# Optimization experiments

Hardware: AMD Instinct MI355X
Metric: run time of the kernel (lower is better)

The kernel has to match this reference:

```python
import jax, jax.numpy as jnp
from jax import lax
import numpy as np

B, C_IN, H, W = 8, 64, 128, 128
C_OUT, K = 64, 3
STRIDE, PAD, DIL = 1, 1, 1
KK = K * K
H_OUT = (H + 2 * PAD - DIL * (K - 1) - 1) // STRIDE + 1
W_OUT = (W + 2 * PAD - DIL * (K - 1) - 1) // STRIDE + 1


def setup_inputs() -> dict:
    key = jax.random.key(0)
    k1, k2, k3, k4 = jax.random.split(key, 4)
    x = jax.random.normal(k1, (B, C_IN, H, W), jnp.float32)
    # offset-predicting conv params (zero-init in the module; use small random
    # values so the deformable sampling path is actually exercised)
    offset_w = jax.random.normal(k2, (2 * KK, C_IN, K, K), jnp.float32) * 0.01
    offset_b = jax.random.normal(k3, (2 * KK,), jnp.float32) * 0.01
    weight = jax.random.normal(k4, (C_OUT, C_IN, K, K), jnp.float32) * (1.0 / np.sqrt(C_IN * KK))
    return {"x": x, "offset_w": offset_w, "offset_b": offset_b, "weight": weight}


def reference(x, offset_w, offset_b, weight):
    # 1) predict offsets: [B, 2*K*K, Hout, Wout], layout (dy, dx) per kernel tap
    offset = lax.conv_general_dilated(
        x, offset_w, (STRIDE, STRIDE), ((PAD, PAD), (PAD, PAD)),
        rhs_dilation=(DIL, DIL), dimension_numbers=("NCHW", "OIHW", "NCHW"))
    offset = offset + offset_b[None, :, None, None]
    off = offset.reshape(B, KK, 2, H_OUT, W_OUT)
    dy = off[:, :, 0].transpose(0, 2, 3, 1)  # [B, Hout, Wout, KK]
    dx = off[:, :, 1].transpose(0, 2, 3, 1)

    # 2) absolute sampling positions p = base_grid + learned offset
    ki, kj = jnp.meshgrid(jnp.arange(K), jnp.arange(K), indexing="ij")
    ki = ki.reshape(-1)
    kj = kj.reshape(-1)
    base_y = (jnp.arange(H_OUT) * STRIDE - PAD)[:, None, None] + ki[None, None, :] * DIL
    base_x = (jnp.arange(W_OUT) * STRIDE - PAD)[None, :, None] + kj[None, None, :] * DIL
    py = base_y[None].astype(x.dtype) + dy  # [B, Hout, Wout, KK]
    px = base_x[None].astype(x.dtype) + dx

    y0 = jnp.floor(py)
    x0 = jnp.floor(px)
    wy1 = py - y0
    wy0 = 1.0 - wy1
    wx1 = px - x0
    wx0 = 1.0 - wx1
    y0i = y0.astype(jnp.int32)
    x0i = x0.astype(jnp.int32)
    y1i = y0i + 1
    x1i = x0i + 1

    L = H_OUT * W_OUT * KK
    f = lambda a: a.reshape(B, L)

    def gather(xb, yi, xi):
        # xb: [C, H, W]; yi, xi: [L] int; zero outside the image
        valid = ((yi >= 0) & (yi < H) & (xi >= 0) & (xi < W)).astype(xb.dtype)
        idx = jnp.clip(yi, 0, H - 1) * W + jnp.clip(xi, 0, W - 1)
        return jnp.take(xb.reshape(C_IN, H * W), idx, axis=1) * valid[None]

    def per_batch(xb, y0i, y1i, x0i, x1i, wy0, wy1, wx0, wx1):
        return (gather(xb, y0i, x0i) * (wy0 * wx0)[None]
                + gather(xb, y0i, x1i) * (wy0 * wx1)[None]
                + gather(xb, y1i, x0i) * (wy1 * wx0)[None]
                + gather(xb, y1i, x1i) * (wy1 * wx1)[None])  # [C, L]

    sampled = jax.vmap(per_batch)(x, f(y0i), f(y1i), f(x0i), f(x1i),
                                  f(wy0), f(wy1), f(wx0), f(wx1))  # [B, C, L]
    sampled = sampled.reshape(B, C_IN, H_OUT, W_OUT, KK)

    # 3) im2col-style contraction against the conv weight (bias=None)
    out = jnp.einsum("bchwk,ock->bohw", sampled, weight.reshape(C_OUT, C_IN, KK))
    return out
```

## Files before the change

kernel.cpp:

```cpp
#include <hip/hip_runtime.h>

#define BATCH 8
#define CIN   64
#define COUT  64
#define HDIM  128
#define WDIM  128
#define HW    (HDIM * WDIM)
#define KK    9

typedef __attribute__((ext_vector_type(8)))  short  short8v;
typedef __attribute__((ext_vector_type(8)))  __bf16 bf16x8;
typedef __attribute__((ext_vector_type(16))) float  f32x16;
typedef float __attribute__((ext_vector_type(2), aligned(4))) float2u;

__device__ __forceinline__ short f2bf(float f) {
    unsigned u = __float_as_uint(f);
    return (short)((u + 0x7fffu + ((u >> 16) & 1u)) >> 16);
}
__device__ __forceinline__ float bf2f(short s) {
    return __uint_as_float(((unsigned)(unsigned short)s) << 16);
}
__device__ __forceinline__ f32x16 mfma_bf16(short8v a, short8v b, f32x16 c) {
    return __builtin_amdgcn_mfma_f32_32x32x16_bf16(
        __builtin_bit_cast(bf16x8, a), __builtin_bit_cast(bf16x8, b), c, 0, 0, 0);
}

__global__ __launch_bounds__(64) void wprep_kernel(
    const float* __restrict__ w, short* __restrict__ Wf)
{
    const int l   = threadIdx.x;
    const int blk = blockIdx.x;
    const int mt  = blk & 1;
    const int s   = blk >> 1;
    const int cg  = s / 9;
    const int t   = s - cg * 9;
    const int oc  = mt * 32 + (l & 31);
    const int cb  = cg * 16 + (l >> 5) * 8;
    short* p0 = Wf + ((size_t)blk * 2 + 0) * 512 + l * 8;
    short* p1 = Wf + ((size_t)blk * 2 + 1) * 512 + l * 8;
#pragma unroll
    for (int e = 0; e < 8; ++e) {
        float v = w[((size_t)oc * CIN + (cb + e)) * KK + t];
        short h = f2bf(v);
        p0[e] = h;
        p1[e] = f2bf(v - bf2f(h));
    }
}

__global__ __launch_bounds__(64) void wprep_off_kernel(
    const float* __restrict__ ow, short* __restrict__ Wo)
{
    const int l  = threadIdx.x;
    const int s  = blockIdx.x;
    const int cg = s / 9;
    const int t  = s - cg * 9;
    const int oc = l & 31;
    const int cb = cg * 16 + (l >> 5) * 8;
    short* p = Wo + (size_t)s * 512 + l * 8;
#pragma unroll
    for (int e = 0; e < 8; ++e) {
        float v = (oc < 18) ? ow[((size_t)oc * CIN + (cb + e)) * KK + t] : 0.0f;
        p[e] = f2bf(v);
    }
}

__global__ __launch_bounds__(256) void offset_conv_kernel(
    const float* __restrict__ x,
    const short* __restrict__ Wo,
    const float* __restrict__ ob,
    float* __restrict__ py,
    float* __restrict__ px)
{
    __shared__ float Xo[3][16][136];

    const int tid = threadIdx.x;
    const int blk = blockIdx.x;
    const int b   = blk & 7;
    const int h   = blk >> 3;
    const int l   = tid & 63;
    const int wv  = tid >> 6;
    const int pcol = 32 * wv + (l & 31);
    const int ch8  = (l >> 5) * 8;

    f32x16 acc;
#pragma unroll
    for (int i = 0; i < 16; ++i) acc[i] = 0.f;

    const float* xb = x + (size_t)b * CIN * HW;

    if (tid < 96) {
        const int r = tid >> 5, cc = (tid >> 1) & 15, side = tid & 1;
        Xo[r][cc][3 + side * 129] = 0.0f;
    }

    auto stage = [&](int cg) {
#pragma unroll
        for (int i = 0; i < 6; ++i) {
            const int f = i * 256 + tid;
            const int r   = f >> 9;
            const int cc  = (f >> 5) & 15;
            const int col = (f & 31) * 4;
            const int y = h - 1 + r;
            float4 v = make_float4(0.f, 0.f, 0.f, 0.f);
            if ((unsigned)y < (unsigned)HDIM)
                v = *(const float4*)(xb + (size_t)(cg * 16 + cc) * HW + y * WDIM + col);
            *(float4*)&Xo[r][cc][4 + col] = v;
        }
    };

    for (int cg = 0; cg < 4; ++cg) {
        __syncthreads();
        stage(cg);
        __syncthreads();

#pragma unroll
        for (int t = 0; t < 9; ++t) {
            const int s = cg * 9 + t;
            const short8v wo = *(const short8v*)(Wo + (size_t)s * 512 + l * 8);

            const int ki = t / 3, kj = t % 3;
            short8v bh;
#pragma unroll
            for (int e = 0; e < 8; ++e)
                bh[e] = f2bf(Xo[ki][ch8 + e][3 + pcol + kj]);

            acc = mfma_bf16(wo, bh, acc);
        }
    }

#pragma unroll
    for (int r = 0; r < 16; ++r) {
        const int oc0 = (r & 3) + 8 * (r >> 2) + 4 * (l >> 5);
        if (oc0 < 18) {
            const int kk = oc0 >> 1, par = oc0 & 1;
            const float base = par ? (float)(pcol - 1 + (kk % 3))
                                   : (float)(h - 1 + (kk / 3));
            float* dst = (par ? px : py)
                       + ((size_t)b * KK + kk) * HW + h * WDIM + pcol;
            *dst = base + acc[r] + ob[oc0];
        }
    }
}

__global__ __launch_bounds__(256)
__attribute__((amdgpu_waves_per_eu(2, 4)))
void deform_mfma_kernel(
    const float* __restrict__ x,
    const short* __restrict__ Wf,
    const float* __restrict__ py,
    const float* __restrict__ px_,
    float* __restrict__ out)
{
    __shared__ float Xw[8][16][128];

    const int tid = threadIdx.x;
    const int blk = blockIdx.x;
    const int b  = blk & 7;
    const int h  = blk >> 3;
    const int l  = tid & 63;
    const int wv = tid >> 6;
    const int mypx = 32 * wv + (l & 31);
    const int ch8  = (l >> 5) * 8;

    f32x16 acc0, acc1;
#pragma unroll
    for (int i = 0; i < 16; ++i) { acc0[i] = 0.f; acc1[i] = 0.f; }

    const float* xb = x + (size_t)b * CIN * HW;
    const float* pyb = py  + (size_t)b * KK * HW + h * WDIM + mypx;
    const float* pxb = px_ + (size_t)b * KK * HW + h * WDIM + mypx;

    auto stage = [&](int cg) {
#pragma unroll
        for (int i = 0; i < 16; ++i) {
            const int f = i * 256 + tid;
            const int r   = f >> 9;
            const int c   = (f >> 5) & 15;
            const int col = (f & 31) * 4;
            const int y = h - 3 + r;
            float4 v = make_float4(0.f, 0.f, 0.f, 0.f);
            if ((unsigned)y < (unsigned)HDIM)
                v = *(const float4*)(xb + (size_t)(cg * 16 + c) * HW + y * WDIM + col);
            *(float4*)&Xw[r][c][col] = v;
        }
    };

    float pyc = pyb[0], pxc = pxb[0];

    for (int cg = 0; cg < 4; ++cg) {
        __syncthreads();
        stage(cg);
        __syncthreads();

        for (int t = 0; t < 9; ++t) {
            const int s = cg * 9 + t;

            const short* wf = Wf + (size_t)(s * 4) * 512;
            const short8v w0h = *(const short8v*)(wf + 0 * 512 + l * 8);
            const short8v w0l = *(const short8v*)(wf + 1 * 512 + l * 8);
            const short8v w1h = *(const short8v*)(wf + 2 * 512 + l * 8);
            const short8v w1l = *(const short8v*)(wf + 3 * 512 + l * 8);

            const float y0f = floorf(pyc), x0f = floorf(pxc);
            const float fy = pyc - y0f, fx = pxc - x0f;
            const int y0 = (int)y0f, x0 = (int)x0f;
            const bool vy0 = (unsigned)y0 < (unsigned)HDIM;
            const bool vy1 = (unsigned)(y0 + 1) < (unsigned)HDIM;
            const bool vx0 = (unsigned)x0 < (unsigned)WDIM;
            const bool vx1 = (unsigned)(x0 + 1) < (unsigned)WDIM;
            const int cy0 = min(max(y0, 0), HDIM - 1);
            const int cy1 = min(max(y0 + 1, 0), HDIM - 1);
            const int axc = min(max(x0, 0), WDIM - 2);
            const float wxL = vx0 ? (1.f - fx) : 0.f;
            const float wxR = vx1 ? fx : 0.f;
            float cgx, cgy;
            if (x0 < 0)              { cgx = wxR; cgy = 0.f; }
            else if (x0 >= WDIM - 1) { cgx = 0.f; cgy = wxL; }
            else                     { cgx = wxL; cgy = wxR; }
            const float wy0v = vy0 ? (1.f - fy) : 0.f;
            const float wy1v = vy1 ? fy : 0.f;
            const float a0  = wy0v * cgx, b0c = wy0v * cgy;
            const float a2  = wy1v * cgx, b2c = wy1v * cgy;

            const int t2 = (t + 1) % 9;
            pyc = pyb[(size_t)t2 * HW];
            pxc = pxb[(size_t)t2 * HW];

            const int r0 = cy0 - (h - 3), r1 = cy1 - (h - 3);
            const bool oob = ((unsigned)r0 > 7u) | ((unsigned)r1 > 7u);

            float v[8];
            if (!oob) {
#pragma unroll
                for (int e = 0; e < 8; ++e) {
                    const float2u p0 = *(const float2u*)&Xw[r0][ch8 + e][axc];
                    const float2u p1 = *(const float2u*)&Xw[r1][ch8 + e][axc];
                    float s0 = p0.x * a0;
                    s0 = fmaf(p0.y, b0c, s0);
                    s0 = fmaf(p1.x, a2,  s0);
                    s0 = fmaf(p1.y, b2c, s0);
                    v[e] = s0;
                }
            } else {
                const int cbase = cg * 16 + ch8;
#pragma unroll
                for (int e = 0; e < 8; ++e) {
                    const float* xc = xb + (size_t)(cbase + e) * HW;
                    float s0 = xc[cy0 * WDIM + axc] * a0;
                    s0 = fmaf(xc[cy0 * WDIM + axc + 1], b0c, s0);
                    s0 = fmaf(xc[cy1 * WDIM + axc],     a2,  s0);
                    s0 = fmaf(xc[cy1 * WDIM + axc + 1], b2c, s0);
                    v[e] = s0;
                }
            }

            short8v bh, bl;
#pragma unroll
            for (int e = 0; e < 8; ++e) {
                const short hs = f2bf(v[e]);
                bh[e] = hs;
                bl[e] = f2bf(v[e] - bf2f(hs));
            }

            acc0 = mfma_bf16(w0h, bh, acc0);
            acc1 = mfma_bf16(w1h, bh, acc1);
            acc0 = mfma_bf16(w0l, bh, acc0);
            acc1 = mfma_bf16(w1l, bh, acc1);
            acc0 = mfma_bf16(w0h, bl, acc0);
            acc1 = mfma_bf16(w1h, bl, acc1);
        }
    }

    float* ob = out + (size_t)b * COUT * HW + h * WDIM + 32 * wv + (l & 31);
#pragma unroll
    for (int r = 0; r < 16; ++r) {
        const int oc0 = (r & 3) + 8 * (r >> 2) + 4 * (l >> 5);
        ob[(size_t)oc0 * HW]        = acc0[r];
        ob[(size_t)(oc0 + 32) * HW] = acc1[r];
    }
}

extern "C" void kernel_launch(void* const* d_in, const int* in_sizes, int n_in,
                              void* d_out, int out_size, void* d_ws, size_t ws_size,
                              hipStream_t stream)
{
    const float* x   = (const float*)d_in[0];
    const float* ow  = (const float*)d_in[1];
    const float* obi = (const float*)d_in[2];
    const float* wgt = (const float*)d_in[3];
    float* out = (float*)d_out;

    float* pyw = (float*)d_ws;
    float* pxw = pyw + (size_t)BATCH * KK * HW;
    short* Wf  = (short*)(pxw + (size_t)BATCH * KK * HW);
    short* Wo  = Wf + (size_t)72 * 2 * 512;

    wprep_kernel<<<dim3(72), 64, 0, stream>>>(wgt, Wf);
    wprep_off_kernel<<<dim3(36), 64, 0, stream>>>(ow, Wo);
    offset_conv_kernel<<<dim3(1024), 256, 0, stream>>>(x, Wo, obi, pyw, pxw);
    deform_mfma_kernel<<<dim3(1024), 256, 0, stream>>>(x, Wf, pyw, pxw, out);
}
```

Before: 183.1 us.

## Fuse offset conv into deformable MFMA kernel and merge weight prep launches

The offset-predicting convolution now runs inside the deformable conv kernel for the same (batch, row) block. It reuses the Xw shared buffer and keeps the sampling positions in LDS, then in registers, so they are never written to and read back from global memory. The two weight-prep kernels are combined into one launch, taking the pipeline from four launches to two. In exchange the fused kernel uses more shared memory and registers, which may lower occupancy, and the offset phase can no longer overlap with other blocks' sampling work the way a separate kernel could.

Result: faster. 174.6 us (-4.7%).

```diff
diff --git a/kernel.cpp b/kernel.cpp
--- a/kernel.cpp
+++ b/kernel.cpp
@@ -25,133 +25,54 @@
         __builtin_bit_cast(bf16x8, a), __builtin_bit_cast(bf16x8, b), c, 0, 0, 0);
 }
 
-__global__ __launch_bounds__(64) void wprep_kernel(
-    const float* __restrict__ w, short* __restrict__ Wf)
+__global__ __launch_bounds__(64) void wprep_all_kernel(
+    const float* __restrict__ w, const float* __restrict__ ow,
+    short* __restrict__ Wf, short* __restrict__ Wo)
 {
     const int l   = threadIdx.x;
     const int blk = blockIdx.x;
-    const int mt  = blk & 1;
-    const int s   = blk >> 1;
-    const int cg  = s / 9;
-    const int t   = s - cg * 9;
-    const int oc  = mt * 32 + (l & 31);
-    const int cb  = cg * 16 + (l >> 5) * 8;
-    short* p0 = Wf + ((size_t)blk * 2 + 0) * 512 + l * 8;
-    short* p1 = Wf + ((size_t)blk * 2 + 1) * 512 + l * 8;
-#pragma unroll
-    for (int e = 0; e < 8; ++e) {
-        float v = w[((size_t)oc * CIN + (cb + e)) * KK + t];
-        short h = f2bf(v);
-        p0[e] = h;
-        p1[e] = f2bf(v - bf2f(h));
-    }
-}
-
-__global__ __launch_bounds__(64) void wprep_off_kernel(
-    const float* __restrict__ ow, short* __restrict__ Wo)
-{
-    const int l  = threadIdx.x;
-    const int s  = blockIdx.x;
-    const int cg = s / 9;
-    const int t  = s - cg * 9;
-    const int oc = l & 31;
-    const int cb = cg * 16 + (l >> 5) * 8;
-    short* p = Wo + (size_t)s * 512 + l * 8;
-#pragma unroll
-    for (int e = 0; e < 8; ++e) {
-        float v = (oc < 18) ? ow[((size_t)oc * CIN + (cb + e)) * KK + t] : 0.0f;
-        p[e] = f2bf(v);
-    }
-}
-
-__global__ __launch_bounds__(256) void offset_conv_kernel(
+    if (blk < 72) {
+        const int mt  = blk & 1;
+        const int s   = blk >> 1;
+        const int cg  = s / 9;
+        const int t   = s - cg * 9;
+        const int oc  = mt * 32 + (l & 31);
+        const int cb  = cg * 16 + (l >> 5) * 8;
+        short* p0 = Wf + ((size_t)blk * 2 + 0) * 512 + l * 8;
+        short* p1 = Wf + ((size_t)blk * 2 + 1) * 512 + l * 8;
+#pragma unroll
+        for (int e = 0; e < 8; ++e) {
+            float v = w[((size_t)oc * CIN + (cb + e)) * KK + t];
+            short h = f2bf(v);
+            p0[e] = h;
+            p1[e] = f2bf(v - bf2f(h));
+        }
+    } else {
+        const int s  = blk - 72;
+        const int cg = s / 9;
+        const int t  = s - cg * 9;
+        const int oc = l & 31;
+        const int cb = cg * 16 + (l >> 5) * 8;
+        short* p = Wo + (size_t)s * 512 + l * 8;
+#pragma unroll
+        for (int e = 0; e < 8; ++e) {
+            float v = (oc < 18) ? ow[((size_t)oc * CIN + (cb + e)) * KK + t] : 0.0f;
+            p[e] = f2bf(v);
+        }
+    }
+}
+
+__global__ __launch_bounds__(256)
+__attribute__((amdgpu_waves_per_eu(2, 4)))
+void fused_deform_kernel(
     const float* __restrict__ x,
+    const short* __restrict__ Wf,
     const short* __restrict__ Wo,
     const float* __restrict__ ob,
-    float* __restrict__ py,
-    float* __restrict__ px)
-{
-    __shared__ float Xo[3][16][136];
-
-    const int tid = threadIdx.x;
-    const int blk = blockIdx.x;
-    const int b   = blk & 7;
-    const int h   = blk >> 3;
-    const int l   = tid & 63;
-    const int wv  = tid >> 6;
-    const int pcol = 32 * wv + (l & 31);
-    const int ch8  = (l >> 5) * 8;
-
-    f32x16 acc;
-#pragma unroll
-    for (int i = 0; i < 16; ++i) acc[i] = 0.f;
-
-    const float* xb = x + (size_t)b * CIN * HW;
-
-    if (tid < 96) {
-        const int r = tid >> 5, cc = (tid >> 1) & 15, side = tid & 1;
-        Xo[r][cc][3 + side * 129] = 0.0f;
-    }
-
-    auto stage = [&](int cg) {
-#pragma unroll
-        for (int i = 0; i < 6; ++i) {
-            const int f = i * 256 + tid;
-            const int r   = f >> 9;
-            const int cc  = (f >> 5) & 15;
-            const int col = (f & 31) * 4;
-            const int y = h - 1 + r;
-            float4 v = make_float4(0.f, 0.f, 0.f, 0.f);
-            if ((unsigned)y < (unsigned)HDIM)
-                v = *(const float4*)(xb + (size_t)(cg * 16 + cc) * HW + y * WDIM + col);
-            *(float4*)&Xo[r][cc][4 + col] = v;
-        }
-    };
-
-    for (int cg = 0; cg < 4; ++cg) {
-        __syncthreads();
-        stage(cg);
-        __syncthreads();
-
-#pragma unroll
-        for (int t = 0; t < 9; ++t) {
-            const int s = cg * 9 + t;
-            const short8v wo = *(const short8v*)(Wo + (size_t)s * 512 + l * 8);
-
-            const int ki = t / 3, kj = t % 3;
-            short8v bh;
-#pragma unroll
-            for (int e = 0; e < 8; ++e)
-                bh[e] = f2bf(Xo[ki][ch8 + e][3 + pcol + kj]);
-
-            acc = mfma_bf16(wo, bh, acc);
-        }
-    }
-
-#pragma unroll
-    for (int r = 0; r < 16; ++r) {
-        const int oc0 = (r & 3) + 8 * (r >> 2) + 4 * (l >> 5);
-        if (oc0 < 18) {
-            const int kk = oc0 >> 1, par = oc0 & 1;
-            const float base = par ? (float)(pcol - 1 + (kk % 3))
-                                   : (float)(h - 1 + (kk / 3));
-            float* dst = (par ? px : py)
-                       + ((size_t)b * KK + kk) * HW + h * WDIM + pcol;
-            *dst = base + acc[r] + ob[oc0];
-        }
-    }
-}
-
-__global__ __launch_bounds__(256)
-__attribute__((amdgpu_waves_per_eu(2, 4)))
-void deform_mfma_kernel(
-    const float* __restrict__ x,
-    const short* __restrict__ Wf,
-    const float* __restrict__ py,
-    const float* __restrict__ px_,
     float* __restrict__ out)
 {
     __shared__ float Xw[8][16][128];
+    __shared__ float pos_lds[18][128];
 
     const int tid = threadIdx.x;
     const int blk = blockIdx.x;
@@ -162,15 +83,75 @@
     const int mypx = 32 * wv + (l & 31);
     const int ch8  = (l >> 5) * 8;
 
+    const float* xb = x + (size_t)b * CIN * HW;
+
+    {
+        float (*Xo)[16][136] = (float(*)[16][136]) & Xw[0][0][0];
+
+        if (tid < 96) {
+            const int r = tid >> 5, cc = (tid >> 1) & 15, side = tid & 1;
+            Xo[r][cc][3 + side * 129] = 0.0f;
+        }
+
+        f32x16 aco;
+#pragma unroll
+        for (int i = 0; i < 16; ++i) aco[i] = 0.f;
+
+        for (int cg = 0; cg < 4; ++cg) {
+            __syncthreads();
+#pragma unroll
+            for (int i = 0; i < 6; ++i) {
+                const int f = i * 256 + tid;
+                const int r   = f >> 9;
+                const int cc  = (f >> 5) & 15;
+                const int col = (f & 31) * 4;
+                const int y = h - 1 + r;
+                float4 v = make_float4(0.f, 0.f, 0.f, 0.f);
+                if ((unsigned)y < (unsigned)HDIM)
+                    v = *(const float4*)(xb + (size_t)(cg * 16 + cc) * HW + y * WDIM + col);
+                *(float4*)&Xo[r][cc][4 + col] = v;
+            }
+            __syncthreads();
+
+#pragma unroll
+            for (int t = 0; t < 9; ++t) {
+                const int s = cg * 9 + t;
+                const short8v wo = *(const short8v*)(Wo + (size_t)s * 512 + l * 8);
+                const int ki = t / 3, kj = t % 3;
+                short8v bh;
+#pragma unroll
+                for (int e = 0; e < 8; ++e)
+                    bh[e] = f2bf(Xo[ki][ch8 + e][3 + mypx + kj]);
+                aco = mfma_bf16(wo, bh, aco);
+            }
+        }
+
+#pragma unroll
+        for (int r = 0; r < 16; ++r) {
+            const int oc0 = (r & 3) + 8 * (r >> 2) + 4 * (l >> 5);
+            if (oc0 < 18) {
+                const int kk = oc0 >> 1, par = oc0 & 1;
+                const float base = par ? (float)(mypx - 1 + (kk % 3))
+                                       : (float)(h - 1 + (kk / 3));
+                pos_lds[oc0][mypx] = base + aco[r] + ob[oc0];
+            }
+        }
+        __syncthreads();
+    }
+
+    float pyr[9], pxr[9];
+#pragma unroll
+    for (int k = 0; k < 9; ++k) {
+        pyr[k] = pos_lds[2 * k][mypx];
+        pxr[k] = pos_lds[2 * k + 1][mypx];
+    }
+
     f32x16 acc0, acc1;
 #pragma unroll
     for (int i = 0; i < 16; ++i) { acc0[i] = 0.f; acc1[i] = 0.f; }
 
-    const float* xb = x + (size_t)b * CIN * HW;
-    const float* pyb = py  + (size_t)b * KK * HW + h * WDIM + mypx;
-    const float* pxb = px_ + (size_t)b * KK * HW + h * WDIM + mypx;
-
-    auto stage = [&](int cg) {
+    for (int cg = 0; cg < 4; ++cg) {
+        __syncthreads();
 #pragma unroll
         for (int i = 0; i < 16; ++i) {
             const int f = i * 256 + tid;
@@ -183,13 +164,6 @@
                 v = *(const float4*)(xb + (size_t)(cg * 16 + c) * HW + y * WDIM + col);
             *(float4*)&Xw[r][c][col] = v;
         }
-    };
-
-    float pyc = pyb[0], pxc = pxb[0];
-
-    for (int cg = 0; cg < 4; ++cg) {
-        __syncthreads();
-        stage(cg);
         __syncthreads();
 
         for (int t = 0; t < 9; ++t) {
@@ -201,6 +175,7 @@
             const short8v w1h = *(const short8v*)(wf + 2 * 512 + l * 8);
             const short8v w1l = *(const short8v*)(wf + 3 * 512 + l * 8);
 
+            const float pyc = pyr[t], pxc = pxr[t];
             const float y0f = floorf(pyc), x0f = floorf(pxc);
             const float fy = pyc - y0f, fx = pxc - x0f;
             const int y0 = (int)y0f, x0 = (int)x0f;
@@ -222,10 +197,6 @@
             const float a0  = wy0v * cgx, b0c = wy0v * cgy;
             const float a2  = wy1v * cgx, b2c = wy1v * cgy;
 
-            const int t2 = (t + 1) % 9;
-            pyc = pyb[(size_t)t2 * HW];
-            pxc = pxb[(size_t)t2 * HW];
-
             const int r0 = cy0 - (h - 3), r1 = cy1 - (h - 3);
             const bool oob = ((unsigned)r0 > 7u) | ((unsigned)r1 > 7u);
 
@@ -271,12 +242,12 @@
         }
     }
 
-    float* ob = out + (size_t)b * COUT * HW + h * WDIM + 32 * wv + (l & 31);
+    float* op = out + (size_t)b * COUT * HW + h * WDIM + 32 * wv + (l & 31);
 #pragma unroll
     for (int r = 0; r < 16; ++r) {
         const int oc0 = (r & 3) + 8 * (r >> 2) + 4 * (l >> 5);
-        ob[(size_t)oc0 * HW]        = acc0[r];
-        ob[(size_t)(oc0 + 32) * HW] = acc1[r];
+        op[(size_t)oc0 * HW]        = acc0[r];
+        op[(size_t)(oc0 + 32) * HW] = acc1[r];
     }
 }
 
@@ -290,13 +261,9 @@
     const float* wgt = (const float*)d_in[3];
     float* out = (float*)d_out;
 
-    float* pyw = (float*)d_ws;
-    float* pxw = pyw + (size_t)BATCH * KK * HW;
-    short* Wf  = (short*)(pxw + (size_t)BATCH * KK * HW);
-    short* Wo  = Wf + (size_t)72 * 2 * 512;
-
-    wprep_kernel<<<dim3(72), 64, 0, stream>>>(wgt, Wf);
-    wprep_off_kernel<<<dim3(36), 64, 0, stream>>>(ow, Wo);
-    offset_conv_kernel<<<dim3(1024), 256, 0, stream>>>(x, Wo, obi, pyw, pxw);
-    deform_mfma_kernel<<<dim3(1024), 256, 0, stream>>>(x, Wf, pyw, pxw, out);
-}
+    short* Wf = (short*)d_ws;
+    short* Wo = Wf + (size_t)72 * 2 * 512;
+
+    wprep_all_kernel<<<dim3(108), 64, 0, stream>>>(wgt, ow, Wf, Wo);
+    fused_deform_kernel<<<dim3(1024), 256, 0, stream>>>(x, Wf, Wo, obi, out);
+}
```
